# Kernel tuning notes

Measured on AMD Instinct MI355X. Metric: run time of the kernel, lower is better.

Reference implementation:

```python
import jax, jax.numpy as jnp
import numpy as np

BATCH, SEQ, DIN, FILTERS, KSIZE = 64, 512, 256, 256, 3

def setup_inputs() -> dict:
    key = jax.random.key(0)
    ks = jax.random.split(key, 5)
    s_u = 1.0 / np.sqrt(DIN)
    return {
        "x": jax.random.normal(ks[0], (BATCH, SEQ, DIN), dtype=jnp.float32),
        "z": jax.random.normal(ks[1], (BATCH, DIN), dtype=jnp.float32),
        "U": jax.random.normal(ks[2], (DIN, DIN), dtype=jnp.float32) * s_u,
        "V": jax.random.normal(ks[3], (DIN, KSIZE * FILTERS), dtype=jnp.float32) * s_u,
        "B_w": jax.random.normal(ks[4], (DIN, KSIZE * FILTERS), dtype=jnp.float32) * s_u,
        "b": jnp.zeros((FILTERS,), dtype=jnp.float32),
        "kernel_size": KSIZE,
    }

def reference(x, z, U, V, B_w, b, kernel_size):
    Bn, L, din = x.shape
    K = int(kernel_size)
    F = V.shape[1] // K
    # per-sample dynamic kernel: (U * sigmoid(z)) @ V + B
    zf = jax.nn.sigmoid(z)                                  # (B, din)
    f = jnp.einsum('de,be,ef->bdf', U, zf, V) + B_w[None]    # (B, din, K*F)
    f = f.reshape(Bn, din, K, F).transpose(0, 2, 1, 3)       # (B, K, din, F)
    # 'same' padding, stride 1
    pad_l, pad_r = (K - 1) // 2, K // 2
    xp = jnp.pad(x, ((0, 0), (pad_l, pad_r), (0, 0)))        # (B, L+K-1, din)
    patches = jnp.stack([xp[:, i:i + L] for i in range(K)], axis=2)  # (B, L, K, din)
    out = jnp.einsum('blkd,bkdf->blf', patches, f) + b       # (B, L, F)
    return jax.nn.relu(out)
```

## Files before the change

### kernel.cpp

```cpp
#include <hip/hip_runtime.h>
#include <math.h>

#define BATCH 64
#define SEQL  512
#define DIN   256
#define NF    256
#define KS    3
#define KF    (KS * NF)

#define XCH 512
#define KC  (KS * XCH)
#define PROWS 130
#define PLD   128
#define PSZ   (PROWS * PLD)

typedef __attribute__((ext_vector_type(8))) short short8;
typedef __attribute__((ext_vector_type(4))) float floatx4;
typedef __attribute__((ext_vector_type(16))) float floatx16;
typedef __attribute__((ext_vector_type(8))) unsigned short ushort8v;

static __device__ __forceinline__ unsigned short f2bf(float f) {
    unsigned int u = __float_as_uint(f);
    return (unsigned short)((u + 0x7FFF + ((u >> 16) & 1)) >> 16);
}

static __device__ __forceinline__ void gl_lds16(const void* g, void* l) {
    __builtin_amdgcn_global_load_lds(
        (const __attribute__((address_space(1))) unsigned int*)g,
        (__attribute__((address_space(3))) unsigned int*)l, 16, 0, 0);
}

__global__ __launch_bounds__(256) void pack_kernel(
    const float* __restrict__ U, const float* __restrict__ V,
    const float* __restrict__ Bw,
    unsigned short* __restrict__ WcT, unsigned short* __restrict__ UT)
{
    const int blk = blockIdx.x;
    const int t   = threadIdx.x;
    __shared__ unsigned short tile[64][64 + 2];

    if (blk < 96) {
        const int f0 = (blk & 3) * 64, c0 = (blk >> 2) * 64;
        const int fl = t & 63, cb = t >> 6;
        #pragma unroll
        for (int it = 0; it < 16; ++it) {
            const int cl = cb + it * 4;
            const int c  = c0 + cl;
            const int k  = c >> 9, ch = c & (XCH - 1);
            const float v = (ch < DIN) ? Bw[(size_t)ch * KF + k * NF + f0 + fl]
                                       : V[(size_t)(ch - DIN) * KF + k * NF + f0 + fl];
            tile[cl][fl] = f2bf(v);
        }
        __syncthreads();
        const int cl2 = t & 63, fb = t >> 6;
        #pragma unroll
        for (int it = 0; it < 16; ++it) {
            const int fl2 = fb + it * 4;
            WcT[(size_t)(f0 + fl2) * KC + c0 + cl2] = tile[cl2][fl2];
        }
    } else {
        const int bb = blk - 96;
        const int e0 = (bb & 3) * 64, d0 = (bb >> 2) * 64;
        const int el = t & 63, db = t >> 6;
        #pragma unroll
        for (int it = 0; it < 16; ++it) {
            const int dl = db + it * 4;
            tile[dl][el] = f2bf(U[(size_t)(d0 + dl) * DIN + e0 + el]);
        }
        __syncthreads();
        const int dl2 = t & 63, eb = t >> 6;
        #pragma unroll
        for (int it = 0; it < 16; ++it) {
            const int el2 = eb + it * 4;
            UT[(size_t)(e0 + el2) * DIN + d0 + dl2] = tile[dl2][el2];
        }
    }
}

__global__ __launch_bounds__(512, 2) void fused_kernel(
    const float* __restrict__ x, const float* __restrict__ z,
    const unsigned short* __restrict__ UT,
    const unsigned short* __restrict__ WcT,
    const float* __restrict__ bias, float* __restrict__ out)
{
    __shared__ __align__(16) unsigned short lds[4 * PSZ];

    const int tid  = threadIdx.x;
    const int lane = tid & 63;
    const int wave = tid >> 6;
    const int quad = lane >> 4, l16 = lane & 15;
    const int l32  = lane & 31, hi  = lane >> 5;
    const int r8   = lane >> 3, ud8 = lane & 7;

    const int bid   = blockIdx.x;
    const int b     = bid >> 2;
    const int lbase = (bid & 3) * 128;

    const int wr = wave >> 2, wc = wave & 3;

    floatx16 acc[2][2] = {};

    auto convBuf = [&](int r) -> unsigned short* {
        return (r < 12) ? (lds + 2 * PSZ + ((r & 1) ? 16384 : 0))
                        : (lds + ((r & 1) ? PSZ : 0));
    };
    auto stageB = [&](int r) {
        unsigned short* buf = convBuf(r);
        const int g = r / 6, k = (r / 2) % 3, hh = r & 1;
        const unsigned short* gW = WcT + (size_t)k * XCH + g * 128 + hh * 64;
        #pragma unroll
        for (int c = 0; c < 4; ++c) {
            const int rr = wave * 32 + c * 8 + r8;
            gl_lds16(gW + (size_t)rr * KC + ((ud8 ^ (rr & 7)) << 3),
                     buf + (size_t)(wave * 32 + c * 8) * 64);
        }
    };
    auto convRegion = [&](int r) {
        const unsigned short* buf = convBuf(r);
        const int g = r / 6, k = (r / 2) % 3, hh = r & 1;
        const unsigned short* P = lds + (size_t)g * PSZ;
        #pragma unroll
        for (int ks = 0; ks < 4; ++ks) {
            short8 af[2], bf[2];
            const int uwa = hh * 8 + ks * 2 + hi;
            #pragma unroll
            for (int i = 0; i < 2; ++i) {
                const int m = wr * 64 + i * 32 + l32 + k;
                af[i] = *(const short8*)&P[m * PLD + ((uwa ^ (m & 15)) << 3)];
            }
            const int uwb = ks * 2 + hi;
            #pragma unroll
            for (int j = 0; j < 2; ++j) {
                const int n = wc * 64 + j * 32 + l32;
                bf[j] = *(const short8*)&buf[n * 64 + ((uwb ^ (n & 7)) << 3)];
            }
            #pragma unroll
            for (int i = 0; i < 2; ++i)
                #pragma unroll
                for (int j = 0; j < 2; ++j)
                    acc[i][j] = __builtin_amdgcn_mfma_f32_32x32x16_bf16(
                        af[i], bf[j], acc[i][j], 0, 0, 0);
        }
    };

    #pragma unroll 1
    for (int p = 0; p < 2; ++p) {
        unsigned short* P = lds + (size_t)p * PSZ;
        #pragma unroll
        for (int it = 0; it < 5; ++it) {
            const int idx = tid + it * 512;
            if (idx < PROWS * 16) {
                const int row = idx >> 4, u = idx & 15;
                const int l = lbase - 1 + row;
                ushort8v h = {};
                if (l >= 0 && l < SEQL) {
                    const float* xp = x + ((size_t)b * SEQL + l) * DIN + p * 128 + u * 8;
                    const float4 v0 = *(const float4*)xp;
                    const float4 v1 = *(const float4*)(xp + 4);
                    h[0] = f2bf(v0.x); h[1] = f2bf(v0.y);
                    h[2] = f2bf(v0.z); h[3] = f2bf(v0.w);
                    h[4] = f2bf(v1.x); h[5] = f2bf(v1.y);
                    h[6] = f2bf(v1.z); h[7] = f2bf(v1.w);
                }
                *(ushort8v*)&P[row * PLD + ((u ^ (row & 15)) << 3)] = h;
            }
        }
    }

    stageB(0);
    __syncthreads();
    #pragma unroll 1
    for (int r = 0; r < 12; ++r) {
        if (r < 11) stageB(r + 1);
        convRegion(r);
        __syncthreads();
    }

    {
        floatx4 accY[9] = {};
        auto utBuf = [&](int rg) -> unsigned short* {
            return lds + 3 * PSZ + ((rg & 1) ? 8192 : 0);
        };
        auto stageU = [&](int rg) {
            unsigned short* buf = utBuf(rg);
            const int eh = rg >> 2, kk = rg & 3;
            const unsigned short* gU = UT + (size_t)(eh * 128) * DIN + kk * 64;
            #pragma unroll
            for (int c = 0; c < 2; ++c) {
                const int rr = wave * 16 + c * 8 + r8;
                gl_lds16(gU + (size_t)rr * DIN + ((ud8 ^ (rr & 7)) << 3),
                         buf + (size_t)(wave * 16 + c * 8) * 64);
            }
        };
        stageU(0);
        __syncthreads();
        #pragma unroll 1
        for (int rg = 0; rg < 8; ++rg) {
            if (rg < 7) stageU(rg + 1);
            const unsigned short* buf = utBuf(rg);
            const int kk = rg & 3;
            const unsigned short* P = lds + (size_t)(kk >> 1) * PSZ;
            const int dh = kk & 1;
            #pragma unroll
            for (int ks = 0; ks < 2; ++ks) {
                const short8 bfv = *(const short8*)
                    &buf[(wave * 16 + l16) * 64 + (((ks * 4 + quad) ^ (l16 & 7)) << 3)];
                #pragma unroll
                for (int i = 0; i < 9; ++i) {
                    const int row = i * 16 + l16;
                    const short8 afv = *(const short8*)
                        &P[row * PLD + (((dh * 8 + ks * 4 + quad) ^ (row & 15)) << 3)];
                    accY[i] = __builtin_amdgcn_mfma_f32_16x16x32_bf16(
                        afv, bfv, accY[i], 0, 0, 0);
                }
            }
            if (rg == 3) {
                const int ecol = wave * 16 + l16;
                const float zf = 1.0f / (1.0f + expf(-z[(size_t)b * DIN + ecol]));
                unsigned short* PY = lds + 2 * PSZ;
                const int u16e = ecol >> 3;
                #pragma unroll
                for (int i = 0; i < 9; ++i)
                    #pragma unroll
                    for (int rr2 = 0; rr2 < 4; ++rr2) {
                        const int row = i * 16 + quad * 4 + rr2;
                        if (row < PROWS)
                            PY[row * PLD + ((u16e ^ (row & 15)) << 3) + (ecol & 7)] =
                                f2bf(accY[i][rr2] * zf);
                    }
                #pragma unroll
                for (int i = 0; i < 9; ++i)
                    #pragma unroll
                    for (int rr2 = 0; rr2 < 4; ++rr2)
                        accY[i][rr2] = 0.0f;
            }
            __syncthreads();
        }
        {
            const int ecol = wave * 16 + l16;
            const float zf = 1.0f / (1.0f + expf(-z[(size_t)b * DIN + 128 + ecol]));
            unsigned short* PY = lds + 3 * PSZ;
            const int u16e = ecol >> 3;
            #pragma unroll
            for (int i = 0; i < 9; ++i)
                #pragma unroll
                for (int rr2 = 0; rr2 < 4; ++rr2) {
                    const int row = i * 16 + quad * 4 + rr2;
                    if (row < PROWS)
                        PY[row * PLD + ((u16e ^ (row & 15)) << 3) + (ecol & 7)] =
                            f2bf(accY[i][rr2] * zf);
                }
        }
    }

    stageB(12);
    __syncthreads();
    #pragma unroll 1
    for (int r = 12; r < 24; ++r) {
        if (r < 23) stageB(r + 1);
        convRegion(r);
        __syncthreads();
    }

    #pragma unroll
    for (int j = 0; j < 2; ++j) {
        const int f  = wc * 64 + j * 32 + l32;
        const float bv = bias[f];
        #pragma unroll
        for (int i = 0; i < 2; ++i) {
            #pragma unroll
            for (int reg = 0; reg < 16; ++reg) {
                const int rowl = wr * 64 + i * 32 + (reg & 3) + 8 * (reg >> 2) + 4 * hi;
                const float v = acc[i][j][reg] + bv;
                out[((size_t)b * SEQL + lbase + rowl) * NF + f] = fmaxf(v, 0.0f);
            }
        }
    }
}

extern "C" void kernel_launch(void* const* d_in, const int* in_sizes, int n_in,
                              void* d_out, int out_size, void* d_ws, size_t ws_size,
                              hipStream_t stream) {
    const float* x    = (const float*)d_in[0];
    const float* z    = (const float*)d_in[1];
    const float* U    = (const float*)d_in[2];
    const float* V    = (const float*)d_in[3];
    const float* Bw   = (const float*)d_in[4];
    const float* bias = (const float*)d_in[5];

    unsigned short* WcT = (unsigned short*)d_ws;
    unsigned short* UT  = WcT + (size_t)NF * KC;
    float* out = (float*)d_out;

    pack_kernel<<<dim3(112), 256, 0, stream>>>(U, V, Bw, WcT, UT);
    fused_kernel<<<dim3(256), 512, 0, stream>>>(x, z, UT, WcT, bias, out);
}
```

Before: 129.3 us.

## Fuse both U-projection halves into one pass and raise MFMA wave priority

The X@U^T projection no longer runs as two sequential halves of four stages each. It now runs as four stages that compute both 128-column halves together, keeping two accumulator sets so each A fragment read from LDS feeds two MFMAs. This halves the A-operand LDS reads and the number of barriers in that phase. s_setprio raises wave priority around the MFMA loops, and the x-loading loop is fully unrolled. The trade-off is a larger staging buffer for U and doubled accumulator registers, which may reduce occupancy or cause spills.

```diff
diff --git a/kernel.cpp b/kernel.cpp
--- a/kernel.cpp
+++ b/kernel.cpp
@@ -119,6 +119,7 @@
         const unsigned short* buf = convBuf(r);
         const int g = r / 6, k = (r / 2) % 3, hh = r & 1;
         const unsigned short* P = lds + (size_t)g * PSZ;
+        __builtin_amdgcn_s_setprio(1);
         #pragma unroll
         for (int ks = 0; ks < 4; ++ks) {
             short8 af[2], bf[2];
@@ -141,9 +142,10 @@
                     acc[i][j] = __builtin_amdgcn_mfma_f32_32x32x16_bf16(
                         af[i], bf[j], acc[i][j], 0, 0, 0);
         }
+        __builtin_amdgcn_s_setprio(0);
     };
 
-    #pragma unroll 1
+    #pragma unroll
     for (int p = 0; p < 2; ++p) {
         unsigned short* P = lds + (size_t)p * PSZ;
         #pragma unroll
@@ -177,69 +179,58 @@
     }
 
     {
-        floatx4 accY[9] = {};
-        auto utBuf = [&](int rg) -> unsigned short* {
-            return lds + 3 * PSZ + ((rg & 1) ? 8192 : 0);
+        floatx4 accY[2][9] = {};
+        auto utBuf = [&](int kk) -> unsigned short* {
+            return lds + 2 * PSZ + ((kk & 1) ? 16384 : 0);
         };
-        auto stageU = [&](int rg) {
-            unsigned short* buf = utBuf(rg);
-            const int eh = rg >> 2, kk = rg & 3;
-            const unsigned short* gU = UT + (size_t)(eh * 128) * DIN + kk * 64;
-            #pragma unroll
-            for (int c = 0; c < 2; ++c) {
-                const int rr = wave * 16 + c * 8 + r8;
+        auto stageU = [&](int kk) {
+            unsigned short* buf = utBuf(kk);
+            const unsigned short* gU = UT + (size_t)kk * 64;
+            #pragma unroll
+            for (int c = 0; c < 4; ++c) {
+                const int rr = wave * 32 + c * 8 + r8;
                 gl_lds16(gU + (size_t)rr * DIN + ((ud8 ^ (rr & 7)) << 3),
-                         buf + (size_t)(wave * 16 + c * 8) * 64);
+                         buf + (size_t)(wave * 32 + c * 8) * 64);
             }
         };
         stageU(0);
         __syncthreads();
         #pragma unroll 1
-        for (int rg = 0; rg < 8; ++rg) {
-            if (rg < 7) stageU(rg + 1);
-            const unsigned short* buf = utBuf(rg);
-            const int kk = rg & 3;
+        for (int kk = 0; kk < 4; ++kk) {
+            if (kk < 3) stageU(kk + 1);
+            const unsigned short* buf = utBuf(kk);
             const unsigned short* P = lds + (size_t)(kk >> 1) * PSZ;
             const int dh = kk & 1;
+            __builtin_amdgcn_s_setprio(1);
             #pragma unroll
             for (int ks = 0; ks < 2; ++ks) {
-                const short8 bfv = *(const short8*)
-                    &buf[(wave * 16 + l16) * 64 + (((ks * 4 + quad) ^ (l16 & 7)) << 3)];
+                short8 bfv[2];
+                #pragma unroll
+                for (int eh = 0; eh < 2; ++eh) {
+                    const int n = eh * 128 + wave * 16 + l16;
+                    bfv[eh] = *(const short8*)
+                        &buf[n * 64 + (((ks * 4 + quad) ^ (n & 7)) << 3)];
+                }
                 #pragma unroll
                 for (int i = 0; i < 9; ++i) {
                     const int row = i * 16 + l16;
                     const short8 afv = *(const short8*)
                         &P[row * PLD + (((dh * 8 + ks * 4 + quad) ^ (row & 15)) << 3)];
-                    accY[i] = __builtin_amdgcn_mfma_f32_16x16x32_bf16(
-                        afv, bfv, accY[i], 0, 0, 0);
-                }
-            }
-            if (rg == 3) {
-                const int ecol = wave * 16 + l16;
-                const float zf = 1.0f / (1.0f + expf(-z[(size_t)b * DIN + ecol]));
-                unsigned short* PY = lds + 2 * PSZ;
-                const int u16e = ecol >> 3;
-                #pragma unroll
-                for (int i = 0; i < 9; ++i)
                     #pragma unroll
-                    for (int rr2 = 0; rr2 < 4; ++rr2) {
-                        const int row = i * 16 + quad * 4 + rr2;
-                        if (row < PROWS)
-                            PY[row * PLD + ((u16e ^ (row & 15)) << 3) + (ecol & 7)] =
-                                f2bf(accY[i][rr2] * zf);
-                    }
-                #pragma unroll
-                for (int i = 0; i < 9; ++i)
-                    #pragma unroll
-                    for (int rr2 = 0; rr2 < 4; ++rr2)
-                        accY[i][rr2] = 0.0f;
-            }
+                    for (int eh = 0; eh < 2; ++eh)
+                        accY[eh][i] = __builtin_amdgcn_mfma_f32_16x16x32_bf16(
+                            afv, bfv[eh], accY[eh][i], 0, 0, 0);
+                }
+            }
+            __builtin_amdgcn_s_setprio(0);
             __syncthreads();
         }
-        {
+        #pragma unroll
+        for (int eh = 0; eh < 2; ++eh) {
             const int ecol = wave * 16 + l16;
-            const float zf = 1.0f / (1.0f + expf(-z[(size_t)b * DIN + 128 + ecol]));
-            unsigned short* PY = lds + 3 * PSZ;
+            const float zf = 1.0f /
+                (1.0f + expf(-z[(size_t)b * DIN + eh * 128 + ecol]));
+            unsigned short* PY = lds + (size_t)(2 + eh) * PSZ;
             const int u16e = ecol >> 3;
             #pragma unroll
             for (int i = 0; i < 9; ++i)
@@ -248,7 +239,7 @@
                     const int row = i * 16 + quad * 4 + rr2;
                     if (row < PROWS)
                         PY[row * PLD + ((u16e ^ (row & 15)) << 3) + (ecol & 7)] =
-                            f2bf(accY[i][rr2] * zf);
+                            f2bf(accY[eh][i][rr2] * zf);
                 }
         }
     }
```

Measured after the change: 128.4 us. No clear change (-0.7%).
